# Kernel optimization log

Hardware: AMD Instinct MI355X
Metric: run time of the kernel (lower is better)

The kernel has to match this reference:

```python
import jax, jax.numpy as jnp
import numpy as np


def setup_inputs() -> dict:
    key = jax.random.key(0)
    k1, k2, k3 = jax.random.split(key, 3)
    B, H, S, D = 4, 16, 1024, 64
    return {
        "query": jax.random.normal(k1, (B, H, S, D), dtype=jnp.float32),
        "key": jax.random.normal(k2, (B, H, D, S), dtype=jnp.float32),  # pre-transposed K
        "scale_factor": 8,  # sqrt(head_dim)
        "attention_mask": jnp.zeros((S, S), dtype=jnp.float32),
        "value": jax.random.normal(k3, (B, H, S, D), dtype=jnp.float32),
    }


def reference(query, key, scale_factor, attention_mask, value):
    # Batched equivalent of the per-(b,h) Python loop:
    # scores = Q @ K^T / scale + mask; probs = softmax(scores); out = probs @ V
    scores = jnp.matmul(query, key) / scale_factor  # [B,H,S,S]
    if attention_mask is not None:
        scores = scores + attention_mask  # broadcast [S,S] over [B,H,S,S]
    probs = jax.nn.softmax(scores, axis=-1)
    return jnp.matmul(probs, value)  # [B,H,S,D]
```

## Files before the change

### kernel.cpp

```cpp
#include <hip/hip_runtime.h>

#define BH  64
#define SEQ 1024
#define DIM 64
#define KT  64

typedef __attribute__((ext_vector_type(8))) short  short8;
typedef __attribute__((ext_vector_type(4))) float  floatx4;

__device__ __forceinline__ ushort f2bf(float x) {
    union { float f; uint u; } v; v.f = x;
    uint r = v.u + 0x7FFFu + ((v.u >> 16) & 1u);
    return (ushort)(r >> 16);
}
__device__ __forceinline__ uint pack2(float lo, float hi) {
    return (uint)f2bf(lo) | ((uint)f2bf(hi) << 16);
}
__device__ __forceinline__ void gld_lds16(const void* g, void* l) {
    __builtin_amdgcn_global_load_lds(
        (const __attribute__((address_space(1))) unsigned int*)g,
        (__attribute__((address_space(3))) unsigned int*)l, 16, 0, 0);
}


__global__ __launch_bounds__(256) void prep_k_kernel(
    const float* __restrict__ in, ushort* __restrict__ out)
{
    __shared__ float tile[32][33];
    const int head = blockIdx.z;
    const int c0 = blockIdx.x * 32;
    const int r0 = blockIdx.y * 32;
    const float* ip = in + (size_t)head * DIM * SEQ;
    char* op = (char*)(out + (size_t)head * SEQ * DIM);
    const int tx = threadIdx.x & 31, ty = threadIdx.x >> 5;
#pragma unroll
    for (int i = 0; i < 4; ++i)
        tile[ty + 8 * i][tx] = ip[(size_t)(r0 + ty + 8 * i) * SEQ + c0 + tx];
    __syncthreads();
#pragma unroll
    for (int i = 0; i < 4; ++i) {
        const int s = c0 + ty + 8 * i;
        const int d = r0 + tx;
        *(ushort*)(op + (size_t)s * 128 + (((d >> 3) ^ (s & 7)) * 16) + (d & 7) * 2)
            = f2bf(tile[tx][ty + 8 * i]);
    }
}

__global__ __launch_bounds__(256) void prep_v_kernel(
    const float* __restrict__ in, ushort* __restrict__ out)
{
    __shared__ float tile[32][33];
    const int head = blockIdx.z;
    const int c0 = blockIdx.x * 32;
    const int r0 = blockIdx.y * 32;
    const float* ip = in + (size_t)head * SEQ * DIM;
    char* op = (char*)(out + (size_t)head * SEQ * DIM);
    const int tx = threadIdx.x & 31, ty = threadIdx.x >> 5;
#pragma unroll
    for (int i = 0; i < 4; ++i)
        tile[ty + 8 * i][tx] = ip[(size_t)(r0 + ty + 8 * i) * DIM + c0 + tx];
    __syncthreads();
#pragma unroll
    for (int i = 0; i < 4; ++i) {
        const int d = c0 + ty + 8 * i;
        const int s = r0 + tx;
        *(ushort*)(op + (size_t)(s >> 6) * 8192 + (size_t)d * 128
                      + ((((s & 63) >> 3) ^ (d & 7)) * 16) + (s & 7) * 2)
            = f2bf(tile[tx][ty + 8 * i]);
    }
}

__global__ __launch_bounds__(256, 5) void mha_mfma2_kernel(
    const float*  __restrict__ Q,
    const ushort* __restrict__ Kbf,
    const int*    __restrict__ scale_p,
    const float*  __restrict__ mask,
    const ushort* __restrict__ Vbf,
    float*        __restrict__ O)
{
    __shared__ __align__(16) ushort Ks[KT * 64];
    __shared__ __align__(16) ushort Vt[DIM * 64];
    __shared__ __align__(16) ushort Ps[4 * 16 * 64];

    const int t    = threadIdx.x;
    const int lane = t & 63, w = t >> 6;
    const int li   = lane & 15, quad = lane >> 4;
    const int lx   = li & 7;
    const int bh   = blockIdx.x >> 4;
    const int q0   = (blockIdx.x & 15) * 64;

    const float inv_scale = 1.0f / (float)scale_p[0];

    {
        const float* Qg = Q + ((size_t)bh * SEQ + q0) * DIM;
        const int rr = t >> 4, cc = (t & 15) * 4;
#pragma unroll
        for (int i = 0; i < 4; ++i) {
            const int row = rr + 16 * i;
            float4 v = *(const float4*)(Qg + (size_t)row * DIM + cc);
            uint2 pw; pw.x = pack2(v.x, v.y); pw.y = pack2(v.z, v.w);
            *(uint2*)((char*)Ks + row * 128 + (((cc >> 3) ^ (row & 7)) * 16)
                      + (cc & 7) * 2) = pw;
        }
    }
    __syncthreads();
    const char* qrow = (const char*)Ks + (w * 16 + li) * 128;
    const short8 qa0 = *(const short8*)(qrow + ((quad ^ lx) * 16));
    const short8 qa1 = *(const short8*)(qrow + (((4 + quad) ^ lx) * 16));

    floatx4 o[4] = {floatx4{0,0,0,0}, floatx4{0,0,0,0},
                    floatx4{0,0,0,0}, floatx4{0,0,0,0}};
    float l_r[4] = {0.f, 0.f, 0.f, 0.f};

    const char* KgH = (const char*)(Kbf + (size_t)bh * SEQ * DIM);
    const char* VgH = (const char*)(Vbf + (size_t)bh * SEQ * DIM);
    const int so = w * 2048 + lane * 16;
    char* ksd = (char*)Ks + w * 2048;
    char* vtd = (char*)Vt + w * 2048;
    char* psw = (char*)Ps + w * 2048;

    const float* mrow = mask + (size_t)(q0 + w * 16 + quad * 4) * SEQ + li;

    for (int kt = 0; kt < SEQ / KT; ++kt) {
        const int key0 = kt * KT;
        __syncthreads();
        const char* kg = KgH + kt * 8192 + so;
        const char* vg = VgH + kt * 8192 + so;
        gld_lds16(kg,        ksd);
        gld_lds16(kg + 1024, ksd + 1024);
        gld_lds16(vg,        vtd);
        gld_lds16(vg + 1024, vtd + 1024);
        __syncthreads();

        float mv[16];
#pragma unroll
        for (int n = 0; n < 4; ++n)
#pragma unroll
            for (int r = 0; r < 4; ++r)
                mv[n * 4 + r] = mrow[(size_t)r * SEQ + key0 + n * 16];

        floatx4 c[4] = {floatx4{0,0,0,0}, floatx4{0,0,0,0},
                        floatx4{0,0,0,0}, floatx4{0,0,0,0}};
#pragma unroll
        for (int n = 0; n < 4; ++n) {
            const char* krow = (const char*)Ks + (n * 16 + li) * 128;
            short8 b0 = *(const short8*)(krow + ((quad ^ lx) * 16));
            short8 b1 = *(const short8*)(krow + (((4 + quad) ^ lx) * 16));
            c[n] = __builtin_amdgcn_mfma_f32_16x16x32_bf16(qa0, b0, c[n], 0, 0, 0);
            c[n] = __builtin_amdgcn_mfma_f32_16x16x32_bf16(qa1, b1, c[n], 0, 0, 0);
        }

#pragma unroll
        for (int n = 0; n < 4; ++n)
#pragma unroll
            for (int r = 0; r < 4; ++r) {
                float s = fminf(fmaf(c[n][r], inv_scale, mv[n * 4 + r]), 80.f);
                float p = __expf(s);
                l_r[r] += p;
                const int row = quad * 4 + r, col = n * 16 + li;
                *(ushort*)(psw + row * 128 + (((col >> 3) ^ (row & 7)) * 16)
                           + (col & 7) * 2) = f2bf(p);
            }

#pragma unroll
        for (int kk = 0; kk < 2; ++kk) {
            short8 a = *(const short8*)(psw + li * 128 + (((kk * 4 + quad) ^ lx) * 16));
#pragma unroll
            for (int n = 0; n < 4; ++n) {
                const char* vrow = (const char*)Vt + (n * 16 + li) * 128;
                short8 b = *(const short8*)(vrow + (((kk * 4 + quad) ^ lx) * 16));
                o[n] = __builtin_amdgcn_mfma_f32_16x16x32_bf16(a, b, o[n], 0, 0, 0);
            }
        }
    }

#pragma unroll
    for (int off = 1; off < 16; off <<= 1)
#pragma unroll
        for (int r = 0; r < 4; ++r)
            l_r[r] += __shfl_xor(l_r[r], off);

    float* Og = O + ((size_t)bh * SEQ + q0) * DIM;
#pragma unroll
    for (int r = 0; r < 4; ++r) {
        const float inv_l = 1.0f / l_r[r];
#pragma unroll
        for (int n = 0; n < 4; ++n)
            Og[(size_t)(w * 16 + quad * 4 + r) * DIM + n * 16 + li] = o[n][r] * inv_l;
    }
}

extern "C" void kernel_launch(void* const* d_in, const int* in_sizes, int n_in,
                              void* d_out, int out_size, void* d_ws, size_t ws_size,
                              hipStream_t stream) {
    const float* Q     = (const float*)d_in[0];
    const float* K     = (const float*)d_in[1];
    const int*   scale = (const int*)d_in[2];
    const float* mask  = (const float*)d_in[3];
    const float* V     = (const float*)d_in[4];
    float*       Out   = (float*)d_out;

    ushort* Kbf = (ushort*)d_ws;
    ushort* Vbf = Kbf + (size_t)BH * SEQ * DIM;

    prep_k_kernel<<<dim3(SEQ / 32, DIM / 32, BH), 256, 0, stream>>>(K, Kbf);
    prep_v_kernel<<<dim3(DIM / 32, SEQ / 32, BH), 256, 0, stream>>>(V, Vbf);
    mha_mfma2_kernel<<<dim3(BH * (SEQ / KT)), 256, 0, stream>>>(Q, Kbf, scale, mask, Vbf, Out);
}
```

Baseline: 136.5 us.

## Merge K/V prep kernels, reorder block-to-head mapping, issue mask loads before barrier

Combines the two bf16 conversion/transposition kernels into one launch by indexing K or V blocks on the z dimension, removing one kernel launch. The attention grid now maps consecutive blocks to different heads instead of consecutive query tiles of the same head, which changes L2 locality for K/V. The mask loads are moved ahead of the barrier that waits for the K/V LDS copy, so their global latency overlaps that wait. The head remapping may reduce K/V reuse across co-resident blocks.

```diff
diff --git a/kernel.cpp b/kernel.cpp
--- a/kernel.cpp
+++ b/kernel.cpp
@@ -23,50 +23,45 @@
 }
 
 
-__global__ __launch_bounds__(256) void prep_k_kernel(
-    const float* __restrict__ in, ushort* __restrict__ out)
+__global__ __launch_bounds__(256) void prep_kv_kernel(
+    const float* __restrict__ Kg, const float* __restrict__ Vg,
+    ushort* __restrict__ Kbf, ushort* __restrict__ Vbf)
 {
     __shared__ float tile[32][33];
-    const int head = blockIdx.z;
-    const int c0 = blockIdx.x * 32;
-    const int r0 = blockIdx.y * 32;
-    const float* ip = in + (size_t)head * DIM * SEQ;
-    char* op = (char*)(out + (size_t)head * SEQ * DIM);
+    const int zz = blockIdx.z;
     const int tx = threadIdx.x & 31, ty = threadIdx.x >> 5;
-#pragma unroll
-    for (int i = 0; i < 4; ++i)
-        tile[ty + 8 * i][tx] = ip[(size_t)(r0 + ty + 8 * i) * SEQ + c0 + tx];
-    __syncthreads();
-#pragma unroll
-    for (int i = 0; i < 4; ++i) {
-        const int s = c0 + ty + 8 * i;
-        const int d = r0 + tx;
-        *(ushort*)(op + (size_t)s * 128 + (((d >> 3) ^ (s & 7)) * 16) + (d & 7) * 2)
-            = f2bf(tile[tx][ty + 8 * i]);
-    }
-}
-
-__global__ __launch_bounds__(256) void prep_v_kernel(
-    const float* __restrict__ in, ushort* __restrict__ out)
-{
-    __shared__ float tile[32][33];
-    const int head = blockIdx.z;
-    const int c0 = blockIdx.x * 32;
-    const int r0 = blockIdx.y * 32;
-    const float* ip = in + (size_t)head * SEQ * DIM;
-    char* op = (char*)(out + (size_t)head * SEQ * DIM);
-    const int tx = threadIdx.x & 31, ty = threadIdx.x >> 5;
-#pragma unroll
-    for (int i = 0; i < 4; ++i)
-        tile[ty + 8 * i][tx] = ip[(size_t)(r0 + ty + 8 * i) * DIM + c0 + tx];
-    __syncthreads();
-#pragma unroll
-    for (int i = 0; i < 4; ++i) {
-        const int d = c0 + ty + 8 * i;
-        const int s = r0 + tx;
-        *(ushort*)(op + (size_t)(s >> 6) * 8192 + (size_t)d * 128
-                      + ((((s & 63) >> 3) ^ (d & 7)) * 16) + (s & 7) * 2)
-            = f2bf(tile[tx][ty + 8 * i]);
+    if (zz < BH) {
+        const int c0 = blockIdx.x * 32;
+        const int r0 = blockIdx.y * 32;
+        const float* ip = Kg + (size_t)zz * DIM * SEQ;
+        char* op = (char*)(Kbf + (size_t)zz * SEQ * DIM);
+#pragma unroll
+        for (int i = 0; i < 4; ++i)
+            tile[ty + 8 * i][tx] = ip[(size_t)(r0 + ty + 8 * i) * SEQ + c0 + tx];
+        __syncthreads();
+#pragma unroll
+        for (int i = 0; i < 4; ++i) {
+            const int s = c0 + ty + 8 * i, d = r0 + tx;
+            *(ushort*)(op + (size_t)s * 128 + (((d >> 3) ^ (s & 7)) * 16) + (d & 7) * 2)
+                = f2bf(tile[tx][ty + 8 * i]);
+        }
+    } else {
+        const int head = zz - BH;
+        const int r0 = blockIdx.x * 32;
+        const int c0 = blockIdx.y * 32;
+        const float* ip = Vg + (size_t)head * SEQ * DIM;
+        char* op = (char*)(Vbf + (size_t)head * SEQ * DIM);
+#pragma unroll
+        for (int i = 0; i < 4; ++i)
+            tile[ty + 8 * i][tx] = ip[(size_t)(r0 + ty + 8 * i) * DIM + c0 + tx];
+        __syncthreads();
+#pragma unroll
+        for (int i = 0; i < 4; ++i) {
+            const int d = c0 + ty + 8 * i, s = r0 + tx;
+            *(ushort*)(op + (size_t)(s >> 6) * 8192 + (size_t)d * 128
+                          + ((((s & 63) >> 3) ^ (d & 7)) * 16) + (s & 7) * 2)
+                = f2bf(tile[tx][ty + 8 * i]);
+        }
     }
 }
 
@@ -84,10 +79,9 @@
 
     const int t    = threadIdx.x;
     const int lane = t & 63, w = t >> 6;
-    const int li   = lane & 15, quad = lane >> 4;
-    const int lx   = li & 7;
-    const int bh   = blockIdx.x >> 4;
-    const int q0   = (blockIdx.x & 15) * 64;
+    const int li   = lane & 15, quad = lane >> 4, lx = li & 7;
+    const int bh   = blockIdx.x & 63;
+    const int q0   = (blockIdx.x >> 6) * 64;
 
     const float inv_scale = 1.0f / (float)scale_p[0];
 
@@ -130,7 +124,6 @@
         gld_lds16(kg + 1024, ksd + 1024);
         gld_lds16(vg,        vtd);
         gld_lds16(vg + 1024, vtd + 1024);
-        __syncthreads();
 
         float mv[16];
 #pragma unroll
@@ -138,6 +131,7 @@
 #pragma unroll
             for (int r = 0; r < 4; ++r)
                 mv[n * 4 + r] = mrow[(size_t)r * SEQ + key0 + n * 16];
+        __syncthreads();
 
         floatx4 c[4] = {floatx4{0,0,0,0}, floatx4{0,0,0,0},
                         floatx4{0,0,0,0}, floatx4{0,0,0,0}};
@@ -203,7 +197,6 @@
     ushort* Kbf = (ushort*)d_ws;
     ushort* Vbf = Kbf + (size_t)BH * SEQ * DIM;
 
-    prep_k_kernel<<<dim3(SEQ / 32, DIM / 32, BH), 256, 0, stream>>>(K, Kbf);
-    prep_v_kernel<<<dim3(DIM / 32, SEQ / 32, BH), 256, 0, stream>>>(V, Vbf);
+    prep_kv_kernel<<<dim3(SEQ / 32, DIM / 32, 2 * BH), 256, 0, stream>>>(K, V, Kbf, Vbf);
     mha_mfma2_kernel<<<dim3(BH * (SEQ / KT)), 256, 0, stream>>>(Q, Kbf, scale, mask, Vbf, Out);
 }
```

Measured after the change: 136.8 us. No clear change (+0.2%).
